# Performance work log

Measured on AMD Instinct MI355X. Metric: run time of the kernel, lower is better.

The kernel has to match this reference:

```python
import jax, jax.numpy as jnp
import numpy as np

N_NODES = 50000
N_EDGES = 800000
IN_DIM = 256
HID = 64
HEADS = 4
OUT_DIM = 16
N_GRAPHS = 64
NEG_SLOPE = 0.2


def setup_inputs() -> dict:
    key = jax.random.key(0)
    ks = jax.random.split(key, 16)
    H2 = HID // 2  # conv2 out channels (heads=1, concat=False)
    H4 = HID // 4
    inp = {
        "x": jax.random.normal(ks[0], (N_NODES, IN_DIM), jnp.float32),
        "edge_index": jax.random.randint(ks[1], (2, N_EDGES), 0, N_NODES, jnp.int64),
        "batch": jnp.sort(jax.random.randint(ks[2], (N_NODES,), 0, N_GRAPHS, jnp.int64)),
        # GATConv 1: in=IN_DIM, out=HID, heads=HEADS, concat=True
        "W1": jax.random.normal(ks[3], (IN_DIM, HEADS * HID), jnp.float32) * 0.05,
        "att_src1": jax.random.normal(ks[4], (HEADS, HID), jnp.float32) * 0.1,
        "att_dst1": jax.random.normal(ks[5], (HEADS, HID), jnp.float32) * 0.1,
        "b1": jnp.zeros((HEADS * HID,), jnp.float32),
        # GATConv 2: in=HEADS*HID, out=HID/2, heads=1, concat=False
        "W2": jax.random.normal(ks[6], (HEADS * HID, H2), jnp.float32) * 0.05,
        "att_src2": jax.random.normal(ks[7], (1, H2), jnp.float32) * 0.1,
        "att_dst2": jax.random.normal(ks[8], (1, H2), jnp.float32) * 0.1,
        "b2": jnp.zeros((H2,), jnp.float32),
        "fc1_w": jax.random.normal(ks[9], (H2, H4), jnp.float32) * 0.1,
        "fc1_b": jnp.zeros((H4,), jnp.float32),
        "fc2_w": jax.random.normal(ks[10], (H4, OUT_DIM), jnp.float32) * 0.1,
        "fc2_b": jnp.zeros((OUT_DIM,), jnp.float32),
    }
    return inp


def gat_conv(x, W, att_src, att_dst, bias, src, dst, num_nodes, concat):
    """PyG-style GATConv (eval mode, self-loops already in src/dst)."""
    H, C = att_src.shape
    h = (x @ W).reshape(num_nodes, H, C)          # [N,H,C]
    a_src = (h * att_src).sum(-1)                 # [N,H]
    a_dst = (h * att_dst).sum(-1)                 # [N,H]
    e = jax.nn.leaky_relu(a_src[src] + a_dst[dst], NEG_SLOPE)  # [E,H]
    # segment softmax over destination nodes (self-loops => every segment nonempty)
    emax = jax.ops.segment_max(e, dst, num_segments=num_nodes)
    ex = jnp.exp(e - emax[dst])
    denom = jax.ops.segment_sum(ex, dst, num_segments=num_nodes)
    alpha = ex / (denom[dst] + 1e-16)             # [E,H]
    msg = h[src] * alpha[:, :, None]              # [E,H,C]
    out = jax.ops.segment_sum(msg, dst, num_segments=num_nodes)  # [N,H,C]
    out = out.reshape(num_nodes, H * C) if concat else out.mean(axis=1)
    return out + bias


def reference(x, edge_index, batch, W1, att_src1, att_dst1, b1,
              W2, att_src2, att_dst2, b2, fc1_w, fc1_b, fc2_w, fc2_b):
    num_nodes = x.shape[0]
    loops = jnp.arange(num_nodes, dtype=edge_index.dtype)
    src = jnp.concatenate([edge_index[0], loops])
    dst = jnp.concatenate([edge_index[1], loops])

    h = gat_conv(x, W1, att_src1, att_dst1, b1, src, dst, num_nodes, concat=True)
    h = jax.nn.relu(h)                                 # dropout: eval no-op
    h = gat_conv(h, W2, att_src2, att_dst2, b2, src, dst, num_nodes, concat=False)

    # global mean pool over graphs
    sums = jax.ops.segment_sum(h, batch, num_segments=N_GRAPHS)
    cnts = jax.ops.segment_sum(jnp.ones((num_nodes,), h.dtype), batch, num_segments=N_GRAPHS)
    g = sums / jnp.maximum(cnts, 1.0)[:, None]         # [G, HID/2]

    g = jax.nn.relu(g)
    g = jax.nn.relu(g @ fc1_w + fc1_b)
    g = jax.nn.relu(g @ fc2_w + fc2_b)
    return g
```

## Files before the change

### kernel.cpp

```cpp
#include <hip/hip_runtime.h>
#include <math.h>

#define NEG 0.2f
#define LMAX 1024
#define CAP 1600
typedef unsigned short u16;
typedef unsigned int u32;
typedef __bf16 bf16x8 __attribute__((ext_vector_type(8)));
typedef float f32x4 __attribute__((ext_vector_type(4)));

__device__ __forceinline__ float bf2f(u16 u) {
    union { unsigned i; float f; } x; x.i = ((unsigned)u) << 16; return x.f;
}
__device__ __forceinline__ u16 f2bf(float f) {
    union { float f; unsigned u; } x; x.f = f;
    unsigned r = x.u + 0x7fffu + ((x.u >> 16) & 1u);
    return (u16)(r >> 16);
}

__global__ void zero_i32(int* __restrict__ p, int n) {
    int i = blockIdx.x * blockDim.x + threadIdx.x;
    if (i < n) p[i] = 0;
}

__global__ __launch_bounds__(256) void bkt_scatter_pad(const int* __restrict__ ei,
                                                       int* __restrict__ bktcur,
                                                       u32* __restrict__ ebuf,
                                                       int E, int ET, int NBK) {
    __shared__ int lcnt[LMAX];
    __shared__ int lbase[LMAX];
    int t = threadIdx.x;
    for (int b = t; b < NBK; b += 256) lcnt[b] = 0;
    __syncthreads();
    int base = blockIdx.x * 8192;
    for (int k = 0; k < 32; ++k) {
        int i = base + k * 256 + t;
        if (i < ET) {
            int d = (i < E) ? ei[E + i] : (i - E);
            atomicAdd(&lcnt[d >> 6], 1);
        }
    }
    __syncthreads();
    for (int b = t; b < NBK; b += 256) {
        int c = lcnt[b];
        lbase[b] = c ? (b * CAP + atomicAdd(&bktcur[b], c)) : 0;
    }
    __syncthreads();
    for (int b = t; b < NBK; b += 256) lcnt[b] = 0;
    __syncthreads();
    for (int k = 0; k < 32; ++k) {
        int i = base + k * 256 + t;
        if (i < ET) {
            int s, d;
            if (i < E) { s = ei[i]; d = ei[E + i]; }
            else       { s = i - E; d = s; }
            int b = d >> 6;
            int idx = atomicAdd(&lcnt[b], 1);
            ebuf[lbase[b] + idx] = (u32)s | ((u32)(d & 63) << 16);
        }
    }
}

__global__ __launch_bounds__(256) void bucket_csr_pad(const u32* __restrict__ ebuf,
                                                      const int* __restrict__ bktcur,
                                                      int* __restrict__ row_ptr,
                                                      int* __restrict__ rowend,
                                                      int* __restrict__ col, int N) {
    __shared__ int cnt[64];
    __shared__ int cur[64];
    int b = blockIdx.x, t = threadIdx.x;
    int v0 = b << 6;
    int s0 = b * CAP, s1 = s0 + bktcur[b];
    if (t < 64) cnt[t] = 0;
    __syncthreads();
    for (int i = s0 + t; i < s1; i += 256)
        atomicAdd(&cnt[(ebuf[i] >> 16) & 63], 1);
    __syncthreads();
    if (t < 64) {
        int c = cnt[t];
        int val = c;
#pragma unroll
        for (int off = 1; off < 64; off <<= 1) {
            int n = __shfl_up(val, off, 64);
            if (t >= off) val += n;
        }
        int excl = s0 + val - c;
        if (v0 + t < N) { row_ptr[v0 + t] = excl; rowend[v0 + t] = excl + c; }
        cur[t] = excl;
    }
    __syncthreads();
    for (int i = s0 + t; i < s1; i += 256) {
        u32 v = ebuf[i];
        int pos = atomicAdd(&cur[(v >> 16) & 63], 1);
        col[pos] = (int)(v & 0xFFFFu);
    }
}

__global__ void prep_w1(const float* __restrict__ W1, const float* __restrict__ att_s,
                        const float* __restrict__ att_d, u16* __restrict__ w1x) {
    int k = blockIdx.x;
    int c = threadIdx.x;
    float w = W1[k * 256 + c];
    w1x[c * 256 + k] = f2bf(w);
    int head = c >> 6;
    float vs = w * att_s[c];
    float vd = w * att_d[c];
#pragma unroll
    for (int mask = 1; mask < 64; mask <<= 1) {
        vs += __shfl_xor(vs, mask, 64);
        vd += __shfl_xor(vd, mask, 64);
    }
    if ((c & 63) == 0) {
        w1x[(256 + head) * 256 + k] = f2bf(vs);
        w1x[(260 + head) * 256 + k] = f2bf(vd);
        w1x[(264 + head) * 256 + k] = 0;
        w1x[(268 + head) * 256 + k] = 0;
    }
}

__global__ void prep_w2(const float* __restrict__ W2, const float* __restrict__ att_s,
                        const float* __restrict__ att_d, u16* __restrict__ w2x) {
    int k = threadIdx.x;
    float a_s = 0.f, a_d = 0.f;
#pragma unroll
    for (int j = 0; j < 32; ++j) {
        float w = W2[k * 32 + j];
        w2x[j * 256 + k] = f2bf(w);
        a_s += w * att_s[j];
        a_d += w * att_d[j];
    }
    w2x[32 * 256 + k] = f2bf(a_s);
    w2x[33 * 256 + k] = f2bf(a_d);
#pragma unroll
    for (int r = 34; r < 48; ++r) w2x[r * 256 + k] = 0;
}

__global__ __launch_bounds__(512) void gemm1_lds(const float* __restrict__ x,
                                                 const u16* __restrict__ w1x,
                                                 u16* __restrict__ h1b,
                                                 float* __restrict__ asad, int N) {
    __shared__ __align__(16) u16 wl[272 * 264];
    for (int f = threadIdx.x; f < 272 * 32; f += 512) {
        int r = f >> 5, cc = f & 31;
        *reinterpret_cast<uint4*>(&wl[r * 264 + cc * 8]) =
            *reinterpret_cast<const uint4*>(w1x + r * 256 + cc * 8);
    }
    __syncthreads();

    int wave = threadIdx.x >> 6, lane = threadIdx.x & 63;
    int g = lane >> 4, l15 = lane & 15;
    int ntiles = (N + 15) >> 4;
    for (int tile = blockIdx.x * 8 + wave; tile < ntiles; tile += gridDim.x * 8) {
        int r0 = tile << 4;
        int arow = r0 + l15; if (arow > N - 1) arow = N - 1;
        const float* xp = x + (size_t)arow * 256 + g * 8;

        f32x4 acc[17];
#pragma unroll
        for (int n = 0; n < 17; ++n) acc[n] = (f32x4){0.f, 0.f, 0.f, 0.f};

#pragma unroll
        for (int ks = 0; ks < 8; ++ks) {
            float4 a0 = *reinterpret_cast<const float4*>(xp + ks * 32);
            float4 a1 = *reinterpret_cast<const float4*>(xp + ks * 32 + 4);
            bf16x8 af;
            af[0] = (__bf16)a0.x; af[1] = (__bf16)a0.y; af[2] = (__bf16)a0.z; af[3] = (__bf16)a0.w;
            af[4] = (__bf16)a1.x; af[5] = (__bf16)a1.y; af[6] = (__bf16)a1.z; af[7] = (__bf16)a1.w;
#pragma unroll
            for (int n = 0; n < 17; ++n) {
                bf16x8 bf = *reinterpret_cast<const bf16x8*>(&wl[(n * 16 + l15) * 264 + ks * 32 + g * 8]);
                acc[n] = __builtin_amdgcn_mfma_f32_16x16x32_bf16(af, bf, acc[n], 0, 0, 0);
            }
        }

#pragma unroll
        for (int reg = 0; reg < 4; ++reg) {
            int grow = r0 + g * 4 + reg;
            if (grow < N) {
#pragma unroll
                for (int n = 0; n < 16; ++n)
                    h1b[(size_t)grow * 256 + n * 16 + l15] = f2bf(acc[n][reg]);
                if (l15 < 8) asad[(size_t)grow * 8 + l15] = acc[16][reg];
            }
        }
    }
}

__global__ __launch_bounds__(256) void conv1_fused(const u16* __restrict__ h1b,
                                                   const float* __restrict__ asad,
                                                   const int* __restrict__ row_ptr,
                                                   const int* __restrict__ rowend,
                                                   const int* __restrict__ col,
                                                   const float* __restrict__ b1,
                                                   u16* __restrict__ hin2b, int N) {
    __shared__ float la[4][128][4];
    __shared__ int   lc[4][128];
    int idx = blockIdx.x * blockDim.x + threadIdx.x;
    int v = idx >> 6; if (v > N - 1) v = N - 1;
    int lane = idx & 63;
    int node = threadIdx.x >> 6;
    int head = lane >> 4, l15 = lane & 15;
    float adst = asad[(size_t)v * 8 + 4 + head];
    int beg = row_ptr[v], end = rowend[v];
    int deg = end - beg;
    bool fast = (deg <= 128);
    float m = -1e30f, l = 0.f;
    if (fast) {
        float e[8]; int u[8];
#pragma unroll
        for (int i = 0; i < 8; ++i) {
            int p = beg + l15 + i * 16;
            float ev = -1e30f; int uu = 0;
            if (p < end) {
                uu = col[p];
                float tv = asad[(size_t)uu * 8 + head] + adst;
                ev = tv > 0.f ? tv : NEG * tv;
            }
            e[i] = ev; u[i] = uu;
        }
        m = e[0];
#pragma unroll
        for (int i = 1; i < 8; ++i) m = fmaxf(m, e[i]);
#pragma unroll
        for (int mask = 1; mask < 16; mask <<= 1) m = fmaxf(m, __shfl_xor(m, mask, 64));
#pragma unroll
        for (int i = 0; i < 8; ++i) {
            int j = l15 + i * 16;
            if (beg + j < end) {
                float a = __expf(e[i] - m);
                l += a;
                la[node][j][head] = a;
                if (head == 0) lc[node][j] = u[i];
            }
        }
#pragma unroll
        for (int mask = 1; mask < 16; mask <<= 1) l += __shfl_xor(l, mask, 64);
    } else {
        for (int p = beg + l15; p < end; p += 16) {
            float tv = asad[(size_t)col[p] * 8 + head] + adst;
            tv = tv > 0.f ? tv : NEG * tv;
            m = fmaxf(m, tv);
        }
#pragma unroll
        for (int mask = 1; mask < 16; mask <<= 1) m = fmaxf(m, __shfl_xor(m, mask, 64));
        for (int p = beg + l15; p < end; p += 16) {
            float tv = asad[(size_t)col[p] * 8 + head] + adst;
            tv = tv > 0.f ? tv : NEG * tv;
            l += __expf(tv - m);
        }
#pragma unroll
        for (int mask = 1; mask < 16; mask <<= 1) l += __shfl_xor(l, mask, 64);
    }
    __syncthreads();
    float inv = 1.f / (l + 1e-16f);

    float ax = 0.f, ay = 0.f, az = 0.f, aw = 0.f;
    if (fast) {
        int j = 0;
        for (; j + 3 < deg; j += 4) {
            float a0 = la[node][j + 0][head];
            float a1 = la[node][j + 1][head];
            float a2 = la[node][j + 2][head];
            float a3 = la[node][j + 3][head];
            int u0 = lc[node][j + 0], u1 = lc[node][j + 1];
            int u2 = lc[node][j + 2], u3 = lc[node][j + 3];
            ushort4 h0 = *reinterpret_cast<const ushort4*>(h1b + (size_t)u0 * 256 + lane * 4);
            ushort4 h1 = *reinterpret_cast<const ushort4*>(h1b + (size_t)u1 * 256 + lane * 4);
            ushort4 h2 = *reinterpret_cast<const ushort4*>(h1b + (size_t)u2 * 256 + lane * 4);
            ushort4 h3 = *reinterpret_cast<const ushort4*>(h1b + (size_t)u3 * 256 + lane * 4);
            ax += a0 * bf2f(h0.x) + a1 * bf2f(h1.x) + a2 * bf2f(h2.x) + a3 * bf2f(h3.x);
            ay += a0 * bf2f(h0.y) + a1 * bf2f(h1.y) + a2 * bf2f(h2.y) + a3 * bf2f(h3.y);
            az += a0 * bf2f(h0.z) + a1 * bf2f(h1.z) + a2 * bf2f(h2.z) + a3 * bf2f(h3.z);
            aw += a0 * bf2f(h0.w) + a1 * bf2f(h1.w) + a2 * bf2f(h2.w) + a3 * bf2f(h3.w);
        }
        for (; j < deg; ++j) {
            float a = la[node][j][head];
            int u = lc[node][j];
            ushort4 hv = *reinterpret_cast<const ushort4*>(h1b + (size_t)u * 256 + lane * 4);
            ax += a * bf2f(hv.x);
            ay += a * bf2f(hv.y);
            az += a * bf2f(hv.z);
            aw += a * bf2f(hv.w);
        }
    } else {
        for (int p = beg; p < end; ++p) {
            int u = col[p];
            float tv = asad[(size_t)u * 8 + head] + adst;
            tv = tv > 0.f ? tv : NEG * tv;
            float a = __expf(tv - m);
            ushort4 hv = *reinterpret_cast<const ushort4*>(h1b + (size_t)u * 256 + lane * 4);
            ax += a * bf2f(hv.x);
            ay += a * bf2f(hv.y);
            az += a * bf2f(hv.z);
            aw += a * bf2f(hv.w);
        }
    }
    int c = lane * 4;
    ushort4 o;
    o.x = f2bf(fmaxf(ax * inv + b1[c + 0], 0.f));
    o.y = f2bf(fmaxf(ay * inv + b1[c + 1], 0.f));
    o.z = f2bf(fmaxf(az * inv + b1[c + 2], 0.f));
    o.w = f2bf(fmaxf(aw * inv + b1[c + 3], 0.f));
    *reinterpret_cast<ushort4*>(hin2b + (size_t)v * 256 + c) = o;
}

__global__ __launch_bounds__(512) void gemm2_mfma(const u16* __restrict__ hin2b,
                                                  const u16* __restrict__ w2x,
                                                  u16* __restrict__ h2b,
                                                  float* __restrict__ as2,
                                                  float* __restrict__ ad2, int N) {
    __shared__ __align__(16) u16 wl[48 * 264];
    for (int f = threadIdx.x; f < 48 * 32; f += 512) {
        int r = f >> 5, cc = f & 31;
        *reinterpret_cast<uint4*>(&wl[r * 264 + cc * 8]) =
            *reinterpret_cast<const uint4*>(w2x + r * 256 + cc * 8);
    }
    __syncthreads();

    int wave = threadIdx.x >> 6, lane = threadIdx.x & 63;
    int g = lane >> 4, l15 = lane & 15;
    int ntiles = (N + 15) >> 4;
    for (int tile = blockIdx.x * 8 + wave; tile < ntiles; tile += gridDim.x * 8) {
        int r0 = tile << 4;
        int arow = r0 + l15; if (arow > N - 1) arow = N - 1;
        const u16* hp = hin2b + (size_t)arow * 256 + g * 8;

        f32x4 acc[3];
#pragma unroll
        for (int n = 0; n < 3; ++n) acc[n] = (f32x4){0.f, 0.f, 0.f, 0.f};

#pragma unroll
        for (int ks = 0; ks < 8; ++ks) {
            bf16x8 af = *reinterpret_cast<const bf16x8*>(hp + ks * 32);
#pragma unroll
            for (int n = 0; n < 3; ++n) {
                bf16x8 bf = *reinterpret_cast<const bf16x8*>(&wl[(n * 16 + l15) * 264 + ks * 32 + g * 8]);
                acc[n] = __builtin_amdgcn_mfma_f32_16x16x32_bf16(af, bf, acc[n], 0, 0, 0);
            }
        }

#pragma unroll
        for (int reg = 0; reg < 4; ++reg) {
            int grow = r0 + g * 4 + reg;
            if (grow < N) {
                h2b[(size_t)grow * 32 + l15]      = f2bf(acc[0][reg]);
                h2b[(size_t)grow * 32 + 16 + l15] = f2bf(acc[1][reg]);
                if (l15 == 0) as2[grow] = acc[2][reg];
                if (l15 == 1) ad2[grow] = acc[2][reg];
            }
        }
    }
}

__global__ __launch_bounds__(256) void conv2_fused(const u16* __restrict__ h2b,
                                                   const float* __restrict__ as2,
                                                   const float* __restrict__ ad2,
                                                   const int* __restrict__ row_ptr,
                                                   const int* __restrict__ rowend,
                                                   const int* __restrict__ col,
                                                   const float* __restrict__ b2,
                                                   float* __restrict__ out2, int N) {
    __shared__ float la[8][128];
    __shared__ int   lc[8][128];
    int idx = blockIdx.x * blockDim.x + threadIdx.x;
    int v = idx >> 5; if (v > N - 1) v = N - 1;
    int lane = idx & 31;
    int node = threadIdx.x >> 5;
    float adst = ad2[v];
    int beg = row_ptr[v], end = rowend[v];
    int deg = end - beg;
    bool fast = (deg <= 128);
    float m = -1e30f, l = 0.f;
    if (fast) {
        float e[4]; int u[4];
#pragma unroll
        for (int i = 0; i < 4; ++i) {
            int p = beg + lane + i * 32;
            float ev = -1e30f; int uu = 0;
            if (p < end) {
                uu = col[p];
                float tv = as2[uu] + adst;
                ev = tv > 0.f ? tv : NEG * tv;
            }
            e[i] = ev; u[i] = uu;
        }
        m = fmaxf(fmaxf(e[0], e[1]), fmaxf(e[2], e[3]));
#pragma unroll
        for (int mask = 1; mask < 32; mask <<= 1) m = fmaxf(m, __shfl_xor(m, mask, 64));
#pragma unroll
        for (int i = 0; i < 4; ++i) {
            int j = lane + i * 32;
            if (beg + j < end) {
                float a = __expf(e[i] - m);
                l += a;
                la[node][j] = a;
                lc[node][j] = u[i];
            }
        }
#pragma unroll
        for (int mask = 1; mask < 32; mask <<= 1) l += __shfl_xor(l, mask, 64);
    } else {
        for (int p = beg + lane; p < end; p += 32) {
            float tv = as2[col[p]] + adst;
            tv = tv > 0.f ? tv : NEG * tv;
            m = fmaxf(m, tv);
        }
#pragma unroll
        for (int mask = 1; mask < 32; mask <<= 1) m = fmaxf(m, __shfl_xor(m, mask, 64));
        for (int p = beg + lane; p < end; p += 32) {
            float tv = as2[col[p]] + adst;
            tv = tv > 0.f ? tv : NEG * tv;
            l += __expf(tv - m);
        }
#pragma unroll
        for (int mask = 1; mask < 32; mask <<= 1) l += __shfl_xor(l, mask, 64);
    }
    __syncthreads();
    float inv = 1.f / (l + 1e-16f);

    float acc = 0.f;
    if (fast) {
        int j = 0;
        for (; j + 3 < deg; j += 4) {
            float a0 = la[node][j + 0], a1 = la[node][j + 1];
            float a2 = la[node][j + 2], a3 = la[node][j + 3];
            int u0 = lc[node][j + 0], u1 = lc[node][j + 1];
            int u2 = lc[node][j + 2], u3 = lc[node][j + 3];
            acc += a0 * bf2f(h2b[(size_t)u0 * 32 + lane])
                 + a1 * bf2f(h2b[(size_t)u1 * 32 + lane])
                 + a2 * bf2f(h2b[(size_t)u2 * 32 + lane])
                 + a3 * bf2f(h2b[(size_t)u3 * 32 + lane]);
        }
        for (; j < deg; ++j)
            acc += la[node][j] * bf2f(h2b[(size_t)lc[node][j] * 32 + lane]);
    } else {
        for (int p = beg; p < end; ++p) {
            int u = col[p];
            float tv = as2[u] + adst;
            tv = tv > 0.f ? tv : NEG * tv;
            acc += __expf(tv - m) * bf2f(h2b[(size_t)u * 32 + lane]);
        }
    }
    out2[(size_t)v * 32 + lane] = acc * inv + b2[lane];
}

__global__ __launch_bounds__(256) void pool_fc(const float* __restrict__ out2,
                                               const int* __restrict__ batch,
                                               const float* __restrict__ fc1w,
                                               const float* __restrict__ fc1b,
                                               const float* __restrict__ fc2w,
                                               const float* __restrict__ fc2b,
                                               float* __restrict__ out, int N) {
    int g = blockIdx.x;
    int lo = 0, hi = N;
    while (lo < hi) { int mid = (lo + hi) >> 1; if (batch[mid] < g) lo = mid + 1; else hi = mid; }
    int s = lo;
    lo = 0; hi = N;
    while (lo < hi) { int mid = (lo + hi) >> 1; if (batch[mid] < g + 1) lo = mid + 1; else hi = mid; }
    int e = lo;

    int c = threadIdx.x & 31, grp = threadIdx.x >> 5;
    float sum = 0.f;
    for (int r = s + grp; r < e; r += 8) sum += out2[(size_t)r * 32 + c];
    __shared__ float part[8][32];
    part[grp][c] = sum;
    __syncthreads();
    __shared__ float g0[32];
    if (grp == 0) {
        float tot = 0.f;
#pragma unroll
        for (int q = 0; q < 8; ++q) tot += part[q][c];
        float cnt = (float)(e - s);
        g0[c] = fmaxf(tot / fmaxf(cnt, 1.0f), 0.f);
    }
    __syncthreads();
    __shared__ float z1[16];
    if (threadIdx.x < 16) {
        float a = fc1b[threadIdx.x];
        for (int k = 0; k < 32; ++k) a += g0[k] * fc1w[k * 16 + threadIdx.x];
        z1[threadIdx.x] = fmaxf(a, 0.f);
    }
    __syncthreads();
    if (threadIdx.x < 16) {
        float a = fc2b[threadIdx.x];
        for (int k = 0; k < 16; ++k) a += z1[k] * fc2w[k * 16 + threadIdx.x];
        out[g * 16 + threadIdx.x] = fmaxf(a, 0.f);
    }
}

extern "C" void kernel_launch(void* const* d_in, const int* in_sizes, int n_in,
                              void* d_out, int out_size, void* d_ws, size_t ws_size,
                              hipStream_t stream) {
    const float* x      = (const float*)d_in[0];
    const int*   ei     = (const int*)d_in[1];
    const int*   batch  = (const int*)d_in[2];
    const float* W1     = (const float*)d_in[3];
    const float* att_s1 = (const float*)d_in[4];
    const float* att_d1 = (const float*)d_in[5];
    const float* b1     = (const float*)d_in[6];
    const float* W2     = (const float*)d_in[7];
    const float* att_s2 = (const float*)d_in[8];
    const float* att_d2 = (const float*)d_in[9];
    const float* b2     = (const float*)d_in[10];
    const float* fc1w   = (const float*)d_in[11];
    const float* fc1b   = (const float*)d_in[12];
    const float* fc2w   = (const float*)d_in[13];
    const float* fc2b   = (const float*)d_in[14];
    float* out = (float*)d_out;

    int N = in_sizes[0] / 256;
    int E = in_sizes[1] / 2;
    int ET = E + N;
    int NBK = (N + 63) >> 6;
    int nchunks = (ET + 8191) / 8192;

    char* ws = (char*)d_ws;
    size_t off = 0;
    auto alloc = [&](size_t bytes) { size_t o = off; off = (off + bytes + 255) & ~255ULL; return o; };
    u16*  w1x    = (u16*)(ws + alloc(272 * 256 * 2));
    u16*  w2x    = (u16*)(ws + alloc(48 * 256 * 2));
    u16*  h1b    = (u16*)(ws + alloc((size_t)N * 256 * 2));
    float* asad  = (float*)(ws + alloc((size_t)N * 8 * 4));
    u16*  hin2b  = (u16*)(ws + alloc((size_t)N * 256 * 2));
    u16*  h2b    = (u16*)(ws + alloc((size_t)N * 32 * 2));
    float* as2   = (float*)(ws + alloc((size_t)N * 4));
    float* ad2   = (float*)(ws + alloc((size_t)N * 4));
    float* out2  = (float*)(ws + alloc((size_t)N * 32 * 4));
    int* row_ptr = (int*)(ws + alloc((size_t)N * 4));
    int* rowend  = (int*)(ws + alloc((size_t)N * 4));
    int* col     = (int*)(ws + alloc((size_t)NBK * CAP * 4));
    int* bktcur  = (int*)(ws + alloc((size_t)NBK * 4));
    u32* ebuf    = (u32*)(ws + alloc((size_t)NBK * CAP * 4));
    (void)ws_size; (void)n_in; (void)out_size;

    prep_w1<<<256, 256, 0, stream>>>(W1, att_s1, att_d1, w1x);
    prep_w2<<<1, 256, 0, stream>>>(W2, att_s2, att_d2, w2x);

    zero_i32<<<(NBK + 255) / 256, 256, 0, stream>>>(bktcur, NBK);
    bkt_scatter_pad<<<nchunks, 256, 0, stream>>>(ei, bktcur, ebuf, E, ET, NBK);
    bucket_csr_pad<<<NBK, 256, 0, stream>>>(ebuf, bktcur, row_ptr, rowend, col, N);

    gemm1_lds<<<256, 512, 0, stream>>>(x, w1x, h1b, asad, N);
    conv1_fused<<<(N * 64 + 255) / 256, 256, 0, stream>>>(h1b, asad, row_ptr, rowend, col, b1, hin2b, N);

    gemm2_mfma<<<256, 512, 0, stream>>>(hin2b, w2x, h2b, as2, ad2, N);
    conv2_fused<<<(N * 32 + 255) / 256, 256, 0, stream>>>(h2b, as2, ad2, row_ptr, rowend, col, b2, out2, N);

    pool_fc<<<64, 256, 0, stream>>>(out2, batch, fc1w, fc1b, fc2w, fc2b, out, N);
}
```

Baseline: 199.3 us.

## Keep W1 in registers, double-buffer x tiles in LDS, merge prep kernels

The first GEMM now holds its slice of W1 (two output column tiles plus the attention tile) in registers per wave. It stages bf16-converted x tiles through a double-buffered LDS buffer, so each block works on one 16-row tile at a time, with all 8 waves sharing it and computing different output columns. This removes the repeated LDS reads of the full weight matrix and the large 140KB LDS footprint, and prefetches the next x tile from global memory during compute. The three small prep and zero kernels are merged into one launch to cut launch overhead. The trade-off is more block-wide synchronisation per tile and a heavier register load, since every wave redundantly computes the attention tile.

```diff
diff --git a/kernel.cpp b/kernel.cpp
--- a/kernel.cpp
+++ b/kernel.cpp
@@ -16,11 +16,6 @@
     union { float f; unsigned u; } x; x.f = f;
     unsigned r = x.u + 0x7fffu + ((x.u >> 16) & 1u);
     return (u16)(r >> 16);
-}
-
-__global__ void zero_i32(int* __restrict__ p, int n) {
-    int i = blockIdx.x * blockDim.x + threadIdx.x;
-    if (i < n) p[i] = 0;
 }
 
 __global__ __launch_bounds__(256) void bkt_scatter_pad(const int* __restrict__ ei,
@@ -96,93 +91,133 @@
     }
 }
 
-__global__ void prep_w1(const float* __restrict__ W1, const float* __restrict__ att_s,
-                        const float* __restrict__ att_d, u16* __restrict__ w1x) {
-    int k = blockIdx.x;
-    int c = threadIdx.x;
-    float w = W1[k * 256 + c];
-    w1x[c * 256 + k] = f2bf(w);
-    int head = c >> 6;
-    float vs = w * att_s[c];
-    float vd = w * att_d[c];
-#pragma unroll
-    for (int mask = 1; mask < 64; mask <<= 1) {
-        vs += __shfl_xor(vs, mask, 64);
-        vd += __shfl_xor(vd, mask, 64);
-    }
-    if ((c & 63) == 0) {
-        w1x[(256 + head) * 256 + k] = f2bf(vs);
-        w1x[(260 + head) * 256 + k] = f2bf(vd);
-        w1x[(264 + head) * 256 + k] = 0;
-        w1x[(268 + head) * 256 + k] = 0;
-    }
-}
-
-__global__ void prep_w2(const float* __restrict__ W2, const float* __restrict__ att_s,
-                        const float* __restrict__ att_d, u16* __restrict__ w2x) {
-    int k = threadIdx.x;
-    float a_s = 0.f, a_d = 0.f;
-#pragma unroll
-    for (int j = 0; j < 32; ++j) {
-        float w = W2[k * 32 + j];
-        w2x[j * 256 + k] = f2bf(w);
-        a_s += w * att_s[j];
-        a_d += w * att_d[j];
-    }
-    w2x[32 * 256 + k] = f2bf(a_s);
-    w2x[33 * 256 + k] = f2bf(a_d);
-#pragma unroll
-    for (int r = 34; r < 48; ++r) w2x[r * 256 + k] = 0;
-}
-
-__global__ __launch_bounds__(512) void gemm1_lds(const float* __restrict__ x,
-                                                 const u16* __restrict__ w1x,
-                                                 u16* __restrict__ h1b,
-                                                 float* __restrict__ asad, int N) {
-    __shared__ __align__(16) u16 wl[272 * 264];
-    for (int f = threadIdx.x; f < 272 * 32; f += 512) {
-        int r = f >> 5, cc = f & 31;
-        *reinterpret_cast<uint4*>(&wl[r * 264 + cc * 8]) =
-            *reinterpret_cast<const uint4*>(w1x + r * 256 + cc * 8);
-    }
-    __syncthreads();
-
-    int wave = threadIdx.x >> 6, lane = threadIdx.x & 63;
+__global__ void prep_all(const float* __restrict__ W1, const float* __restrict__ att_s1,
+                         const float* __restrict__ att_d1, u16* __restrict__ w1x,
+                         const float* __restrict__ W2, const float* __restrict__ att_s2,
+                         const float* __restrict__ att_d2, u16* __restrict__ w2x,
+                         int* __restrict__ bktcur, int NBK) {
+    int t = threadIdx.x;
+    if (blockIdx.x < 256) {
+        int k = blockIdx.x;
+        int c = t;
+        float w = W1[k * 256 + c];
+        w1x[c * 256 + k] = f2bf(w);
+        int head = c >> 6;
+        float vs = w * att_s1[c];
+        float vd = w * att_d1[c];
+#pragma unroll
+        for (int mask = 1; mask < 64; mask <<= 1) {
+            vs += __shfl_xor(vs, mask, 64);
+            vd += __shfl_xor(vd, mask, 64);
+        }
+        if ((c & 63) == 0) {
+            w1x[(256 + head) * 256 + k] = f2bf(vs);
+            w1x[(260 + head) * 256 + k] = f2bf(vd);
+            w1x[(264 + head) * 256 + k] = 0;
+            w1x[(268 + head) * 256 + k] = 0;
+        }
+    } else {
+        int k = t;
+        float a_s = 0.f, a_d = 0.f;
+#pragma unroll
+        for (int j = 0; j < 32; ++j) {
+            float w = W2[k * 32 + j];
+            w2x[j * 256 + k] = f2bf(w);
+            a_s += w * att_s2[j];
+            a_d += w * att_d2[j];
+        }
+        w2x[32 * 256 + k] = f2bf(a_s);
+        w2x[33 * 256 + k] = f2bf(a_d);
+#pragma unroll
+        for (int r = 34; r < 48; ++r) w2x[r * 256 + k] = 0;
+        for (int i = t; i < NBK; i += 256) bktcur[i] = 0;
+    }
+}
+
+__global__ __launch_bounds__(512) void gemm1_regw(const float* __restrict__ x,
+                                                  const u16* __restrict__ w1x,
+                                                  u16* __restrict__ h1b,
+                                                  float* __restrict__ asad, int N) {
+    __shared__ __align__(16) u16 xs[2][16][264];
+    int t = threadIdx.x;
+    int wave = t >> 6, lane = t & 63;
     int g = lane >> 4, l15 = lane & 15;
+
+    bf16x8 wreg[3][8];
+#pragma unroll
+    for (int ci = 0; ci < 3; ++ci) {
+        int ct = (ci == 2) ? 16 : (wave * 2 + ci);
+        const u16* wp = w1x + (size_t)(ct * 16 + l15) * 256 + g * 8;
+#pragma unroll
+        for (int ks = 0; ks < 8; ++ks)
+            wreg[ci][ks] = *reinterpret_cast<const bf16x8*>(wp + ks * 32);
+    }
+
+    int srow = t >> 5, sseg = t & 31;
     int ntiles = (N + 15) >> 4;
-    for (int tile = blockIdx.x * 8 + wave; tile < ntiles; tile += gridDim.x * 8) {
-        int r0 = tile << 4;
-        int arow = r0 + l15; if (arow > N - 1) arow = N - 1;
-        const float* xp = x + (size_t)arow * 256 + g * 8;
-
-        f32x4 acc[17];
-#pragma unroll
-        for (int n = 0; n < 17; ++n) acc[n] = (f32x4){0.f, 0.f, 0.f, 0.f};
-
+    int tile0 = blockIdx.x;
+    if (tile0 >= ntiles) return;
+
+    auto stage_load = [&](int tile, float4& a0, float4& a1) {
+        int arow = tile * 16 + srow; if (arow > N - 1) arow = N - 1;
+        const float* xp = x + (size_t)arow * 256 + sseg * 8;
+        a0 = *reinterpret_cast<const float4*>(xp);
+        a1 = *reinterpret_cast<const float4*>(xp + 4);
+    };
+    auto stage_write = [&](int buf, const float4& a0, const float4& a1) {
+        uint4 o;
+        o.x = (unsigned)f2bf(a0.x) | ((unsigned)f2bf(a0.y) << 16);
+        o.y = (unsigned)f2bf(a0.z) | ((unsigned)f2bf(a0.w) << 16);
+        o.z = (unsigned)f2bf(a1.x) | ((unsigned)f2bf(a1.y) << 16);
+        o.w = (unsigned)f2bf(a1.z) | ((unsigned)f2bf(a1.w) << 16);
+        *reinterpret_cast<uint4*>(&xs[buf][srow][sseg * 8]) = o;
+    };
+
+    {
+        float4 a0, a1;
+        stage_load(tile0, a0, a1);
+        stage_write(0, a0, a1);
+    }
+    __syncthreads();
+
+    int cur = 0;
+    for (int tile = tile0; tile < ntiles; tile += 256) {
+        int nxt = tile + 256;
+        bool hasnext = nxt < ntiles;
+        float4 p0, p1;
+        if (hasnext) stage_load(nxt, p0, p1);
+
+        f32x4 acc[3];
+#pragma unroll
+        for (int ci = 0; ci < 3; ++ci) acc[ci] = (f32x4){0.f, 0.f, 0.f, 0.f};
 #pragma unroll
         for (int ks = 0; ks < 8; ++ks) {
-            float4 a0 = *reinterpret_cast<const float4*>(xp + ks * 32);
-            float4 a1 = *reinterpret_cast<const float4*>(xp + ks * 32 + 4);
-            bf16x8 af;
-            af[0] = (__bf16)a0.x; af[1] = (__bf16)a0.y; af[2] = (__bf16)a0.z; af[3] = (__bf16)a0.w;
-            af[4] = (__bf16)a1.x; af[5] = (__bf16)a1.y; af[6] = (__bf16)a1.z; af[7] = (__bf16)a1.w;
-#pragma unroll
-            for (int n = 0; n < 17; ++n) {
-                bf16x8 bf = *reinterpret_cast<const bf16x8*>(&wl[(n * 16 + l15) * 264 + ks * 32 + g * 8]);
-                acc[n] = __builtin_amdgcn_mfma_f32_16x16x32_bf16(af, bf, acc[n], 0, 0, 0);
-            }
-        }
-
-#pragma unroll
-        for (int reg = 0; reg < 4; ++reg) {
-            int grow = r0 + g * 4 + reg;
-            if (grow < N) {
-#pragma unroll
-                for (int n = 0; n < 16; ++n)
-                    h1b[(size_t)grow * 256 + n * 16 + l15] = f2bf(acc[n][reg]);
-                if (l15 < 8) asad[(size_t)grow * 8 + l15] = acc[16][reg];
-            }
-        }
+            bf16x8 bfr = *reinterpret_cast<const bf16x8*>(&xs[cur][l15][ks * 32 + g * 8]);
+#pragma unroll
+            for (int ci = 0; ci < 3; ++ci)
+                acc[ci] = __builtin_amdgcn_mfma_f32_16x16x32_bf16(wreg[ci][ks], bfr, acc[ci], 0, 0, 0);
+        }
+
+        int nrow = tile * 16 + l15;
+        if (nrow < N) {
+#pragma unroll
+            for (int ci = 0; ci < 2; ++ci) {
+                int ct = wave * 2 + ci;
+                ushort4 o;
+                o.x = f2bf(acc[ci][0]); o.y = f2bf(acc[ci][1]);
+                o.z = f2bf(acc[ci][2]); o.w = f2bf(acc[ci][3]);
+                *reinterpret_cast<ushort4*>(h1b + (size_t)nrow * 256 + ct * 16 + g * 4) = o;
+            }
+            if (wave == 0 && g < 2) {
+#pragma unroll
+                for (int reg = 0; reg < 4; ++reg)
+                    asad[(size_t)nrow * 8 + g * 4 + reg] = acc[2][reg];
+            }
+        }
+        __syncthreads();
+        if (hasnext) stage_write(cur ^ 1, p0, p1);
+        __syncthreads();
+        cur ^= 1;
     }
 }
 
@@ -533,14 +568,12 @@
     u32* ebuf    = (u32*)(ws + alloc((size_t)NBK * CAP * 4));
     (void)ws_size; (void)n_in; (void)out_size;
 
-    prep_w1<<<256, 256, 0, stream>>>(W1, att_s1, att_d1, w1x);
-    prep_w2<<<1, 256, 0, stream>>>(W2, att_s2, att_d2, w2x);
-
-    zero_i32<<<(NBK + 255) / 256, 256, 0, stream>>>(bktcur, NBK);
+    prep_all<<<257, 256, 0, stream>>>(W1, att_s1, att_d1, w1x, W2, att_s2, att_d2, w2x, bktcur, NBK);
+
     bkt_scatter_pad<<<nchunks, 256, 0, stream>>>(ei, bktcur, ebuf, E, ET, NBK);
     bucket_csr_pad<<<NBK, 256, 0, stream>>>(ebuf, bktcur, row_ptr, rowend, col, N);
 
-    gemm1_lds<<<256, 512, 0, stream>>>(x, w1x, h1b, asad, N);
+    gemm1_regw<<<256, 512, 0, stream>>>(x, w1x, h1b, asad, N);
     conv1_fused<<<(N * 64 + 255) / 256, 256, 0, stream>>>(h1b, asad, row_ptr, rowend, col, b1, hin2b, N);
 
     gemm2_mfma<<<256, 512, 0, stream>>>(hin2b, w2x, h2b, as2, ad2, N);
```

Result: no change. 196.4 us (-1.5%).
